# Optimization experiments

Hardware: AMD Instinct MI355X
Metric: run time of the kernel (lower is better)

The kernel has to match this reference:

```python
import jax, jax.numpy as jnp
import numpy as np

N, L, D, H, HIST = 4, 1024, 1024, 16, 128
HD = D // H          # head_dim = 64
SCALE = D ** 0.5     # note: original scales by sqrt(model_dim), not sqrt(head_dim)


def _band_mask():
    # get_mask: tril XOR tril(diag=-history_len) -> True inside the causal band.
    # masked_fill fills where mask is True, so pass the complement (True outside band).
    r = jnp.arange(L)[:, None]
    c = jnp.arange(L)[None, :]
    band = (c <= r) & (c > r - HIST)  # band of width HIST incl. diagonal
    return jnp.broadcast_to(~band, (N, 1, L, L))


def setup_inputs() -> dict:
    key = jax.random.key(0)
    ks = jax.random.split(key, 8)
    s = 0.02
    return {
        "values": jax.random.normal(ks[0], (N, L, D), jnp.float32),
        "keys": jax.random.normal(ks[1], (N, L, D), jnp.float32),
        "query": jax.random.normal(ks[2], (N, L, D), jnp.float32),
        "mask": _band_mask(),
        "Wv": jax.random.normal(ks[3], (HD, HD), jnp.float32) * s,
        "Wk": jax.random.normal(ks[4], (HD, HD), jnp.float32) * s,
        "Wq": jax.random.normal(ks[5], (HD, HD), jnp.float32) * s,
        "Wo": jax.random.normal(ks[6], (D, D), jnp.float32) * s,
        "bo": jax.random.normal(ks[7], (D,), jnp.float32) * s,
    }


def reference(values, keys, query, mask, Wv, Wk, Wq, Wo, bo):
    n, qlen, _ = query.shape
    # split heads and apply per-head linear projections (nn.Linear: x @ W.T)
    v = values.reshape(n, -1, H, HD) @ Wv.T
    k = keys.reshape(n, -1, H, HD) @ Wk.T
    q = query.reshape(n, qlen, H, HD) @ Wq.T
    # full energy [n, h, q, k]
    energy = jnp.einsum('nqhd,nkhd->nhqk', q, k)
    energy = jnp.where(mask, jnp.float32(-1e20), energy)
    scores = jax.nn.softmax(energy / SCALE, axis=-1)
    # NOTE: faithful to original einsum 'nhql,nlhd->nlhd' (reduces over q):
    # attention[n,l,h,d] = (sum_q scores[n,h,q,l]) * v[n,l,h,d]
    attention = jnp.einsum('nhql,nlhd->nlhd', scores, v)
    out = attention.reshape(n, qlen, D) @ Wo.T + bo
    return out
```

## Files before the change

kernel.cpp:

```cpp
#include <hip/hip_runtime.h>
#include <hip/hip_bf16.h>
#include <math.h>


using short8 = __attribute__((ext_vector_type(8))) short;
using f32x4  = __attribute__((ext_vector_type(4))) float;

__device__ __forceinline__ unsigned short f2bf(float x) {
    unsigned u = __float_as_uint(x);
    u += 0x7FFFu + ((u >> 16) & 1u);
    return (unsigned short)(u >> 16);
}

__global__ __launch_bounds__(256) void k_stage(const float* __restrict__ keys,
                                               const float* __restrict__ Wq,
                                               const float* __restrict__ Wk,
                                               const float* __restrict__ Wv,
                                               const float4* __restrict__ Wo4,
                                               unsigned short* __restrict__ kk2p,
                                               ushort4* __restrict__ wob4,
                                               unsigned short* __restrict__ Wvb,
                                               float* __restrict__ w) {
    __shared__ unsigned short Ml[64 * 64];

    const int b = blockIdx.x, tid = threadIdx.x;

    if (b < 1024) {
        const int wv = tid >> 6, lane = tid & 63;
        const int m = lane & 15, q4 = lane >> 4, ksel = q4 * 8;

        {
            short8 aM0, aM1;
#pragma unroll
            for (int j = 0; j < 8; ++j) {
                aM0[j] = (short)f2bf(Wq[(ksel + j) * 64 + wv * 16 + m]);
                aM1[j] = (short)f2bf(Wq[(32 + ksel + j) * 64 + wv * 16 + m]);
            }
#pragma unroll
            for (int fc = 0; fc < 4; ++fc) {
                short8 bM0, bM1;
#pragma unroll
                for (int j = 0; j < 8; ++j) {
                    bM0[j] = (short)f2bf(Wk[(ksel + j) * 64 + fc * 16 + m]);
                    bM1[j] = (short)f2bf(Wk[(32 + ksel + j) * 64 + fc * 16 + m]);
                }
                f32x4 a = f32x4{0.f, 0.f, 0.f, 0.f};
                a = __builtin_amdgcn_mfma_f32_16x16x32_bf16(aM0, bM0, a, 0, 0, 0);
                a = __builtin_amdgcn_mfma_f32_16x16x32_bf16(aM1, bM1, a, 0, 0, 0);
#pragma unroll
                for (int r = 0; r < 4; ++r)
                    Ml[(wv * 16 + q4 * 4 + r) * 64 + fc * 16 + m] =
                        f2bf(a[r] * (1.0f / 32.0f));
            }
        }
        __syncthreads();

        const long R0 = (long)b * 64;
        const float* ka = keys + (R0 + wv * 16 + m) * 64;
        short8 af[2];
#pragma unroll
        for (int ch = 0; ch < 2; ++ch) {
            float4 x0 = *reinterpret_cast<const float4*>(ka + ch * 32 + ksel);
            float4 x1 = *reinterpret_cast<const float4*>(ka + ch * 32 + ksel + 4);
            short8 a;
            a[0] = (short)f2bf(x0.x); a[1] = (short)f2bf(x0.y);
            a[2] = (short)f2bf(x0.z); a[3] = (short)f2bf(x0.w);
            a[4] = (short)f2bf(x1.x); a[5] = (short)f2bf(x1.y);
            a[6] = (short)f2bf(x1.z); a[7] = (short)f2bf(x1.w);
            af[ch] = a;
        }

        f32x4 acc[4];
#pragma unroll
        for (int fc = 0; fc < 4; ++fc) {
            acc[fc] = f32x4{0.f, 0.f, 0.f, 0.f};
#pragma unroll
            for (int ch = 0; ch < 2; ++ch) {
                short8 bf = *reinterpret_cast<const short8*>(
                    &Ml[(fc * 16 + m) * 64 + ch * 32 + ksel]);
                acc[fc] = __builtin_amdgcn_mfma_f32_16x16x32_bf16(af[ch], bf, acc[fc], 0, 0, 0);
            }
        }

        const long rowb = R0 + wv * 16 + (lane >> 4) * 4;
#pragma unroll
        for (int reg = 0; reg < 4; ++reg) {
            long rg = rowb + reg;
            int hh = (int)(rg & 15);
            int ll = (int)((rg >> 4) & 1023);
            int nn = (int)(rg >> 14);
            unsigned short* orow = kk2p + ((size_t)((nn * 16 + hh) * 1024 + ll)) * 64;
#pragma unroll
            for (int fc = 0; fc < 4; ++fc)
                orow[fc * 16 + m] = f2bf(acc[fc][reg]);
        }
    } else if (b < 2048) {
        const int bb = b - 1024;
        int idx = bb * 256 + tid;
        float4 v = Wo4[idx];
        ushort4 o; o.x = f2bf(v.x); o.y = f2bf(v.y);
        o.z = f2bf(v.z); o.w = f2bf(v.w);
        wob4[idx] = o;
        if (bb < 256) w[bb * 256 + tid] = 0.f;
    } else {
        int idx = (b - 2048) * 256 + tid;
        Wvb[idx] = f2bf(Wv[idx]);
    }
}

__global__ __launch_bounds__(256) void k_w2(const float* __restrict__ query,
                                            const unsigned short* __restrict__ kk2p,
                                            float* __restrict__ w) {
    __shared__ float wloc[192];

    const int tid  = threadIdx.x;
    const int b    = blockIdx.x;
    const int nh   = b & 63;
    const int tile = b >> 6;
    const int t0   = tile * 64;
    const int h    = nh & 15, n = nh >> 4;

    if (tid < 192) wloc[tid] = 0.f;
    __syncthreads();

    const int wv = tid >> 6, lane = tid & 63;
    const int m = lane & 15, q4 = lane >> 4, ksel = q4 * 8;

    const float* qrow = query +
        ((size_t)(n * 1024 + t0 + wv * 16 + m)) * 1024 + h * 64;
    float4 x0 = *reinterpret_cast<const float4*>(qrow + ksel);
    float4 x1 = *reinterpret_cast<const float4*>(qrow + ksel + 4);
    float4 x2 = *reinterpret_cast<const float4*>(qrow + 32 + ksel);
    float4 x3 = *reinterpret_cast<const float4*>(qrow + 32 + ksel + 4);
    short8 af0, af1;
    af0[0] = (short)f2bf(x0.x); af0[1] = (short)f2bf(x0.y);
    af0[2] = (short)f2bf(x0.z); af0[3] = (short)f2bf(x0.w);
    af0[4] = (short)f2bf(x1.x); af0[5] = (short)f2bf(x1.y);
    af0[6] = (short)f2bf(x1.z); af0[7] = (short)f2bf(x1.w);
    af1[0] = (short)f2bf(x2.x); af1[1] = (short)f2bf(x2.y);
    af1[2] = (short)f2bf(x2.z); af1[3] = (short)f2bf(x2.w);
    af1[4] = (short)f2bf(x3.x); af1[5] = (short)f2bf(x3.y);
    af1[6] = (short)f2bf(x3.z); af1[7] = (short)f2bf(x3.w);

    const unsigned short* kb = kk2p + (size_t)nh * 1024 * 64;

    f32x4 acc[12];
#pragma unroll
    for (int ni = 0; ni < 12; ++ni) {
        int l = t0 - 127 + ni * 16 + m;
        int lc = min(max(l, 0), 1023);
        const unsigned short* kp = kb + (size_t)lc * 64 + ksel;
        short8 b0 = *reinterpret_cast<const short8*>(kp);
        short8 b1 = *reinterpret_cast<const short8*>(kp + 32);
        f32x4 a = f32x4{0.f, 0.f, 0.f, 0.f};
        a = __builtin_amdgcn_mfma_f32_16x16x32_bf16(af0, b0, a, 0, 0, 0);
        a = __builtin_amdgcn_mfma_f32_16x16x32_bf16(af1, b1, a, 0, 0, 0);
        acc[ni] = a;
    }

    const int rbase = wv * 16 + q4 * 4;
    float rs[4] = {0.f, 0.f, 0.f, 0.f};
#pragma unroll
    for (int ni = 0; ni < 12; ++ni) {
        const int c = ni * 16 + m;
#pragma unroll
        for (int reg = 0; reg < 4; ++reg) {
            const int rlw = rbase + reg;
            bool valid = (c >= rlw) && (c <= rlw + 127) && (c + t0 >= 127);
            float e = valid ? __expf(acc[ni][reg]) : 0.f;
            acc[ni][reg] = e;
            rs[reg] += e;
        }
    }
#pragma unroll
    for (int reg = 0; reg < 4; ++reg) {
#pragma unroll
        for (int mm = 1; mm < 16; mm <<= 1) rs[reg] += __shfl_xor(rs[reg], mm);
        rs[reg] = 1.0f / rs[reg];
    }
#pragma unroll
    for (int ni = 0; ni < 12; ++ni) {
        float cs = acc[ni][0] * rs[0] + acc[ni][1] * rs[1] +
                   acc[ni][2] * rs[2] + acc[ni][3] * rs[3];
        cs += __shfl_xor(cs, 16);
        cs += __shfl_xor(cs, 32);
        if (lane < 16) atomicAdd(&wloc[ni * 16 + m], cs);
    }
    __syncthreads();

    for (int c = tid; c < 192; c += 256) {
        int l = t0 - 127 + c;
        if (l >= 0 && l < 1024)
            atomicAdd(&w[(size_t)nh * 1024 + l], wloc[c]);
    }
}

__global__ __launch_bounds__(256) void k_ap2(const float* __restrict__ values,
                                             const unsigned short* __restrict__ Wvb,
                                             const float* __restrict__ w,
                                             unsigned short* __restrict__ apb) {
    const int tid = threadIdx.x;
    const long R0 = (long)blockIdx.x * 64;
    const int wv = tid >> 6, lane = tid & 63;
    const int m = lane & 15, ksel = (lane >> 4) * 8;

    const float* va = values + (R0 + wv * 16 + m) * 64;
    short8 af[2];
#pragma unroll
    for (int ch = 0; ch < 2; ++ch) {
        float4 x0 = *reinterpret_cast<const float4*>(va + ch * 32 + ksel);
        float4 x1 = *reinterpret_cast<const float4*>(va + ch * 32 + ksel + 4);
        short8 a;
        a[0] = (short)f2bf(x0.x); a[1] = (short)f2bf(x0.y);
        a[2] = (short)f2bf(x0.z); a[3] = (short)f2bf(x0.w);
        a[4] = (short)f2bf(x1.x); a[5] = (short)f2bf(x1.y);
        a[6] = (short)f2bf(x1.z); a[7] = (short)f2bf(x1.w);
        af[ch] = a;
    }

    f32x4 acc[4];
#pragma unroll
    for (int dc = 0; dc < 4; ++dc) {
        acc[dc] = f32x4{0.f, 0.f, 0.f, 0.f};
#pragma unroll
        for (int ch = 0; ch < 2; ++ch) {
            short8 bf = *reinterpret_cast<const short8*>(
                Wvb + (size_t)(dc * 16 + m) * 64 + ch * 32 + ksel);
            acc[dc] = __builtin_amdgcn_mfma_f32_16x16x32_bf16(af[ch], bf, acc[dc], 0, 0, 0);
        }
    }

    const long rowb = R0 + wv * 16 + (lane >> 4) * 4;
    float wf[4];
#pragma unroll
    for (int reg = 0; reg < 4; ++reg) {
        long rg = rowb + reg;
        int hh = (int)(rg & 15);
        int ll = (int)((rg >> 4) & 1023);
        int nn = (int)(rg >> 14);
        wf[reg] = w[((size_t)(nn * 16 + hh) << 10) + ll];
    }
#pragma unroll
    for (int dc = 0; dc < 4; ++dc)
#pragma unroll
        for (int reg = 0; reg < 4; ++reg)
            apb[(size_t)(rowb + reg) * 64 + dc * 16 + m] = f2bf(acc[dc][reg] * wf[reg]);
}

__global__ __launch_bounds__(256) void k_out_mfma(
    const unsigned short* __restrict__ apb,
    const unsigned short* __restrict__ wob,
    const float* __restrict__ bo,
    float* __restrict__ out) {
    __shared__ unsigned short As[2][2][128 * 32];
    __shared__ unsigned short Bs[2][2][64 * 32];

    const int tid  = threadIdx.x;
    const int wv   = tid >> 6;
    const int lane = tid & 63;
    const int m    = lane & 15;

    const int by = blockIdx.x & 31;
    const int bx = blockIdx.x >> 5;
    const long arow0 = (long)by * 128;
    const int  bcol0 = bx * 64;

    f32x4 acc[2][4];
#pragma unroll
    for (int mi = 0; mi < 2; ++mi)
#pragma unroll
        for (int ni = 0; ni < 4; ++ni) acc[mi][ni] = f32x4{0.f, 0.f, 0.f, 0.f};

    const int r0s = tid >> 2;
    const int kks = (tid & 3) * 8;

    auto stage = [&](int buf, int kt) {
        const int k0 = kt * 64;
#pragma unroll
        for (int hh = 0; hh < 2; ++hh) {
            const int kh = k0 + hh * 32;
#pragma unroll
            for (int i = 0; i < 2; ++i) {
                const unsigned short* g =
                    apb + (arow0 + i * 64 + r0s) * 1024 + kh + kks;
                __builtin_amdgcn_global_load_lds(
                    (const __attribute__((address_space(1))) unsigned int*)g,
                    (__attribute__((address_space(3))) unsigned int*)&As[buf][hh][i * 2048 + wv * 512],
                    16, 0, 0);
            }
            {
                const unsigned short* g =
                    wob + (size_t)(bcol0 + r0s) * 1024 + kh + kks;
                __builtin_amdgcn_global_load_lds(
                    (const __attribute__((address_space(1))) unsigned int*)g,
                    (__attribute__((address_space(3))) unsigned int*)&Bs[buf][hh][wv * 512],
                    16, 0, 0);
            }
        }
    };

    stage(0, 0);
    __syncthreads();

    int cur = 0;
    for (int kt = 0; kt < 16; ++kt) {
        if (kt < 15) stage(cur ^ 1, kt + 1);

        const int koff = (lane >> 4) * 8;
        const int rA = wv * 32 + m;
        short8 af[2][2], bf[4][2];
#pragma unroll
        for (int hh = 0; hh < 2; ++hh) {
#pragma unroll
            for (int mi = 0; mi < 2; ++mi)
                af[mi][hh] = *reinterpret_cast<const short8*>(
                    &As[cur][hh][(rA + mi * 16) * 32 + koff]);
#pragma unroll
            for (int ni = 0; ni < 4; ++ni)
                bf[ni][hh] = *reinterpret_cast<const short8*>(
                    &Bs[cur][hh][(ni * 16 + m) * 32 + koff]);
        }
#pragma unroll
        for (int mi = 0; mi < 2; ++mi)
#pragma unroll
            for (int ni = 0; ni < 4; ++ni) {
                acc[mi][ni] = __builtin_amdgcn_mfma_f32_16x16x32_bf16(
                    af[mi][0], bf[ni][0], acc[mi][ni], 0, 0, 0);
                acc[mi][ni] = __builtin_amdgcn_mfma_f32_16x16x32_bf16(
                    af[mi][1], bf[ni][1], acc[mi][ni], 0, 0, 0);
            }
        __syncthreads();
        cur ^= 1;
    }

    const int colb = bcol0 + m;
    const int rowb = (int)arow0 + wv * 32 + (lane >> 4) * 4;
#pragma unroll
    for (int ni = 0; ni < 4; ++ni) {
        const int col = colb + ni * 16;
        const float bias = bo[col];
#pragma unroll
        for (int mi = 0; mi < 2; ++mi) {
            const int row = rowb + mi * 16;
#pragma unroll
            for (int r = 0; r < 4; ++r)
                out[(size_t)(row + r) * 1024 + col] = acc[mi][ni][r] + bias;
        }
    }
}

extern "C" void kernel_launch(void* const* d_in, const int* in_sizes, int n_in,
                              void* d_out, int out_size, void* d_ws, size_t ws_size,
                              hipStream_t stream) {
    const float* values = (const float*)d_in[0];
    const float* keys   = (const float*)d_in[1];
    const float* query  = (const float*)d_in[2];
    const float* Wv     = (const float*)d_in[4];
    const float* Wk     = (const float*)d_in[5];
    const float* Wq     = (const float*)d_in[6];
    const float* Wo     = (const float*)d_in[7];
    const float* bo     = (const float*)d_in[8];
    float* out = (float*)d_out;

    float* w             = (float*)d_ws;
    unsigned short* Wvb  = (unsigned short*)(w + 65536);
    unsigned short* wob  = Wvb + 4096;
    unsigned short* kk2p = wob + 1024 * 1024;
    unsigned short* apb  = kk2p + 64 * 1024 * 64;

    k_stage<<<2064, 256, 0, stream>>>(keys, Wq, Wk, Wv, (const float4*)Wo,
                                      kk2p, (ushort4*)wob, Wvb, w);
    k_w2<<<1024, 256, 0, stream>>>(query, kk2p, w);
    k_ap2<<<1024, 256, 0, stream>>>(values, Wvb, w, apb);
    k_out_mfma<<<512, 256, 0, stream>>>(apb, wob, bo, out);
}
```

Baseline: 156.7 us.

## Fuse key projection into score kernel and replace global atomics with partial sums

Merges the key-projection stage into the attention-weight kernel. Each block now recomputes the projected keys for its 192-row band into shared memory instead of reading a precomputed bf16 key buffer from global memory. Column-sum partials are written per block to a workspace, and the value kernel gathers up to three partials per row, which replaces global atomics and the zeroing pass. This removes one launch and the global round trip for the keys. In exchange, each key row is projected about three times and the block uses more shared memory.

Result: faster. 150.4 us (-4.0%).

```diff
diff --git a/kernel.cpp b/kernel.cpp
--- a/kernel.cpp
+++ b/kernel.cpp
@@ -12,22 +12,36 @@
     return (unsigned short)(u >> 16);
 }
 
-__global__ __launch_bounds__(256) void k_stage(const float* __restrict__ keys,
+__global__ __launch_bounds__(256) void k_fused(const float* __restrict__ keys,
+                                               const float* __restrict__ query,
                                                const float* __restrict__ Wq,
                                                const float* __restrict__ Wk,
                                                const float* __restrict__ Wv,
                                                const float4* __restrict__ Wo4,
-                                               unsigned short* __restrict__ kk2p,
+                                               float* __restrict__ wpart,
                                                ushort4* __restrict__ wob4,
-                                               unsigned short* __restrict__ Wvb,
-                                               float* __restrict__ w) {
+                                               unsigned short* __restrict__ Wvb) {
     __shared__ unsigned short Ml[64 * 64];
+    __shared__ unsigned short band[192 * 72];
+    __shared__ float wloc[192];
 
     const int b = blockIdx.x, tid = threadIdx.x;
 
     if (b < 1024) {
+        const int nh = b & 63, tile = b >> 6;
+        const int t0 = tile * 64;
+        const int h = nh & 15, n = nh >> 4;
         const int wv = tid >> 6, lane = tid & 63;
         const int m = lane & 15, q4 = lane >> 4, ksel = q4 * 8;
+
+        if (tid < 192) wloc[tid] = 0.f;
+
+        const float* qrow = query +
+            ((size_t)(n * 1024 + t0 + wv * 16 + m)) * 1024 + h * 64;
+        const float4 x0 = *reinterpret_cast<const float4*>(qrow + ksel);
+        const float4 x1 = *reinterpret_cast<const float4*>(qrow + ksel + 4);
+        const float4 x2 = *reinterpret_cast<const float4*>(qrow + 32 + ksel);
+        const float4 x3 = *reinterpret_cast<const float4*>(qrow + 32 + ksel + 4);
 
         {
             short8 aM0, aM1;
@@ -55,45 +69,96 @@
         }
         __syncthreads();
 
-        const long R0 = (long)b * 64;
-        const float* ka = keys + (R0 + wv * 16 + m) * 64;
-        short8 af[2];
-#pragma unroll
-        for (int ch = 0; ch < 2; ++ch) {
-            float4 x0 = *reinterpret_cast<const float4*>(ka + ch * 32 + ksel);
-            float4 x1 = *reinterpret_cast<const float4*>(ka + ch * 32 + ksel + 4);
-            short8 a;
-            a[0] = (short)f2bf(x0.x); a[1] = (short)f2bf(x0.y);
-            a[2] = (short)f2bf(x0.z); a[3] = (short)f2bf(x0.w);
-            a[4] = (short)f2bf(x1.x); a[5] = (short)f2bf(x1.y);
-            a[6] = (short)f2bf(x1.z); a[7] = (short)f2bf(x1.w);
-            af[ch] = a;
-        }
-
-        f32x4 acc[4];
-#pragma unroll
-        for (int fc = 0; fc < 4; ++fc) {
-            acc[fc] = f32x4{0.f, 0.f, 0.f, 0.f};
+#pragma unroll
+        for (int grp = 0; grp < 3; ++grp) {
+            const int pA = grp * 64 + wv * 16 + m;
+            const int lrow = min(max(t0 - 127 + pA, 0), 1023);
+            const float* ka = keys + ((size_t)(n * 1024 + lrow)) * 1024 + h * 64;
+            short8 af[2];
 #pragma unroll
             for (int ch = 0; ch < 2; ++ch) {
-                short8 bf = *reinterpret_cast<const short8*>(
-                    &Ml[(fc * 16 + m) * 64 + ch * 32 + ksel]);
-                acc[fc] = __builtin_amdgcn_mfma_f32_16x16x32_bf16(af[ch], bf, acc[fc], 0, 0, 0);
-            }
-        }
-
-        const long rowb = R0 + wv * 16 + (lane >> 4) * 4;
+                float4 k0 = *reinterpret_cast<const float4*>(ka + ch * 32 + ksel);
+                float4 k1 = *reinterpret_cast<const float4*>(ka + ch * 32 + ksel + 4);
+                short8 a;
+                a[0] = (short)f2bf(k0.x); a[1] = (short)f2bf(k0.y);
+                a[2] = (short)f2bf(k0.z); a[3] = (short)f2bf(k0.w);
+                a[4] = (short)f2bf(k1.x); a[5] = (short)f2bf(k1.y);
+                a[6] = (short)f2bf(k1.z); a[7] = (short)f2bf(k1.w);
+                af[ch] = a;
+            }
+            f32x4 acc[4];
+#pragma unroll
+            for (int fc = 0; fc < 4; ++fc) {
+                acc[fc] = f32x4{0.f, 0.f, 0.f, 0.f};
+#pragma unroll
+                for (int ch = 0; ch < 2; ++ch) {
+                    short8 bf = *reinterpret_cast<const short8*>(
+                        &Ml[(fc * 16 + m) * 64 + ch * 32 + ksel]);
+                    acc[fc] = __builtin_amdgcn_mfma_f32_16x16x32_bf16(af[ch], bf, acc[fc], 0, 0, 0);
+                }
+            }
+            const int prow = grp * 64 + wv * 16 + q4 * 4;
+#pragma unroll
+            for (int reg = 0; reg < 4; ++reg)
+#pragma unroll
+                for (int fc = 0; fc < 4; ++fc)
+                    band[(prow + reg) * 72 + fc * 16 + m] = f2bf(acc[fc][reg]);
+        }
+        __syncthreads();
+
+        short8 af0, af1;
+        af0[0] = (short)f2bf(x0.x); af0[1] = (short)f2bf(x0.y);
+        af0[2] = (short)f2bf(x0.z); af0[3] = (short)f2bf(x0.w);
+        af0[4] = (short)f2bf(x1.x); af0[5] = (short)f2bf(x1.y);
+        af0[6] = (short)f2bf(x1.z); af0[7] = (short)f2bf(x1.w);
+        af1[0] = (short)f2bf(x2.x); af1[1] = (short)f2bf(x2.y);
+        af1[2] = (short)f2bf(x2.z); af1[3] = (short)f2bf(x2.w);
+        af1[4] = (short)f2bf(x3.x); af1[5] = (short)f2bf(x3.y);
+        af1[6] = (short)f2bf(x3.z); af1[7] = (short)f2bf(x3.w);
+
+        f32x4 acc[12];
+#pragma unroll
+        for (int ni = 0; ni < 12; ++ni) {
+            const unsigned short* kp_ = &band[(ni * 16 + m) * 72 + ksel];
+            short8 b0 = *reinterpret_cast<const short8*>(kp_);
+            short8 b1 = *reinterpret_cast<const short8*>(kp_ + 32);
+            f32x4 a = f32x4{0.f, 0.f, 0.f, 0.f};
+            a = __builtin_amdgcn_mfma_f32_16x16x32_bf16(af0, b0, a, 0, 0, 0);
+            a = __builtin_amdgcn_mfma_f32_16x16x32_bf16(af1, b1, a, 0, 0, 0);
+            acc[ni] = a;
+        }
+
+        const int rbase = wv * 16 + q4 * 4;
+        float rs[4] = {0.f, 0.f, 0.f, 0.f};
+#pragma unroll
+        for (int ni = 0; ni < 12; ++ni) {
+            const int c = ni * 16 + m;
+#pragma unroll
+            for (int reg = 0; reg < 4; ++reg) {
+                const int rlw = rbase + reg;
+                bool valid = (c >= rlw) && (c <= rlw + 127) && (c + t0 >= 127);
+                float e = valid ? __expf(acc[ni][reg]) : 0.f;
+                acc[ni][reg] = e;
+                rs[reg] += e;
+            }
+        }
 #pragma unroll
         for (int reg = 0; reg < 4; ++reg) {
-            long rg = rowb + reg;
-            int hh = (int)(rg & 15);
-            int ll = (int)((rg >> 4) & 1023);
-            int nn = (int)(rg >> 14);
-            unsigned short* orow = kk2p + ((size_t)((nn * 16 + hh) * 1024 + ll)) * 64;
-#pragma unroll
-            for (int fc = 0; fc < 4; ++fc)
-                orow[fc * 16 + m] = f2bf(acc[fc][reg]);
-        }
+#pragma unroll
+            for (int mm = 1; mm < 16; mm <<= 1) rs[reg] += __shfl_xor(rs[reg], mm);
+            rs[reg] = 1.0f / rs[reg];
+        }
+#pragma unroll
+        for (int ni = 0; ni < 12; ++ni) {
+            float cs = acc[ni][0] * rs[0] + acc[ni][1] * rs[1] +
+                       acc[ni][2] * rs[2] + acc[ni][3] * rs[3];
+            cs += __shfl_xor(cs, 16);
+            cs += __shfl_xor(cs, 32);
+            if (lane < 16) atomicAdd(&wloc[ni * 16 + m], cs);
+        }
+        __syncthreads();
+
+        if (tid < 192) wpart[(size_t)b * 192 + tid] = wloc[tid];
     } else if (b < 2048) {
         const int bb = b - 1024;
         int idx = bb * 256 + tid;
@@ -101,103 +166,15 @@
         ushort4 o; o.x = f2bf(v.x); o.y = f2bf(v.y);
         o.z = f2bf(v.z); o.w = f2bf(v.w);
         wob4[idx] = o;
-        if (bb < 256) w[bb * 256 + tid] = 0.f;
     } else {
         int idx = (b - 2048) * 256 + tid;
         Wvb[idx] = f2bf(Wv[idx]);
     }
 }
 
-__global__ __launch_bounds__(256) void k_w2(const float* __restrict__ query,
-                                            const unsigned short* __restrict__ kk2p,
-                                            float* __restrict__ w) {
-    __shared__ float wloc[192];
-
-    const int tid  = threadIdx.x;
-    const int b    = blockIdx.x;
-    const int nh   = b & 63;
-    const int tile = b >> 6;
-    const int t0   = tile * 64;
-    const int h    = nh & 15, n = nh >> 4;
-
-    if (tid < 192) wloc[tid] = 0.f;
-    __syncthreads();
-
-    const int wv = tid >> 6, lane = tid & 63;
-    const int m = lane & 15, q4 = lane >> 4, ksel = q4 * 8;
-
-    const float* qrow = query +
-        ((size_t)(n * 1024 + t0 + wv * 16 + m)) * 1024 + h * 64;
-    float4 x0 = *reinterpret_cast<const float4*>(qrow + ksel);
-    float4 x1 = *reinterpret_cast<const float4*>(qrow + ksel + 4);
-    float4 x2 = *reinterpret_cast<const float4*>(qrow + 32 + ksel);
-    float4 x3 = *reinterpret_cast<const float4*>(qrow + 32 + ksel + 4);
-    short8 af0, af1;
-    af0[0] = (short)f2bf(x0.x); af0[1] = (short)f2bf(x0.y);
-    af0[2] = (short)f2bf(x0.z); af0[3] = (short)f2bf(x0.w);
-    af0[4] = (short)f2bf(x1.x); af0[5] = (short)f2bf(x1.y);
-    af0[6] = (short)f2bf(x1.z); af0[7] = (short)f2bf(x1.w);
-    af1[0] = (short)f2bf(x2.x); af1[1] = (short)f2bf(x2.y);
-    af1[2] = (short)f2bf(x2.z); af1[3] = (short)f2bf(x2.w);
-    af1[4] = (short)f2bf(x3.x); af1[5] = (short)f2bf(x3.y);
-    af1[6] = (short)f2bf(x3.z); af1[7] = (short)f2bf(x3.w);
-
-    const unsigned short* kb = kk2p + (size_t)nh * 1024 * 64;
-
-    f32x4 acc[12];
-#pragma unroll
-    for (int ni = 0; ni < 12; ++ni) {
-        int l = t0 - 127 + ni * 16 + m;
-        int lc = min(max(l, 0), 1023);
-        const unsigned short* kp = kb + (size_t)lc * 64 + ksel;
-        short8 b0 = *reinterpret_cast<const short8*>(kp);
-        short8 b1 = *reinterpret_cast<const short8*>(kp + 32);
-        f32x4 a = f32x4{0.f, 0.f, 0.f, 0.f};
-        a = __builtin_amdgcn_mfma_f32_16x16x32_bf16(af0, b0, a, 0, 0, 0);
-        a = __builtin_amdgcn_mfma_f32_16x16x32_bf16(af1, b1, a, 0, 0, 0);
-        acc[ni] = a;
-    }
-
-    const int rbase = wv * 16 + q4 * 4;
-    float rs[4] = {0.f, 0.f, 0.f, 0.f};
-#pragma unroll
-    for (int ni = 0; ni < 12; ++ni) {
-        const int c = ni * 16 + m;
-#pragma unroll
-        for (int reg = 0; reg < 4; ++reg) {
-            const int rlw = rbase + reg;
-            bool valid = (c >= rlw) && (c <= rlw + 127) && (c + t0 >= 127);
-            float e = valid ? __expf(acc[ni][reg]) : 0.f;
-            acc[ni][reg] = e;
-            rs[reg] += e;
-        }
-    }
-#pragma unroll
-    for (int reg = 0; reg < 4; ++reg) {
-#pragma unroll
-        for (int mm = 1; mm < 16; mm <<= 1) rs[reg] += __shfl_xor(rs[reg], mm);
-        rs[reg] = 1.0f / rs[reg];
-    }
-#pragma unroll
-    for (int ni = 0; ni < 12; ++ni) {
-        float cs = acc[ni][0] * rs[0] + acc[ni][1] * rs[1] +
-                   acc[ni][2] * rs[2] + acc[ni][3] * rs[3];
-        cs += __shfl_xor(cs, 16);
-        cs += __shfl_xor(cs, 32);
-        if (lane < 16) atomicAdd(&wloc[ni * 16 + m], cs);
-    }
-    __syncthreads();
-
-    for (int c = tid; c < 192; c += 256) {
-        int l = t0 - 127 + c;
-        if (l >= 0 && l < 1024)
-            atomicAdd(&w[(size_t)nh * 1024 + l], wloc[c]);
-    }
-}
-
 __global__ __launch_bounds__(256) void k_ap2(const float* __restrict__ values,
                                              const unsigned short* __restrict__ Wvb,
-                                             const float* __restrict__ w,
+                                             const float* __restrict__ wpart,
                                              unsigned short* __restrict__ apb) {
     const int tid = threadIdx.x;
     const long R0 = (long)blockIdx.x * 64;
@@ -238,7 +215,12 @@
         int hh = (int)(rg & 15);
         int ll = (int)((rg >> 4) & 1023);
         int nn = (int)(rg >> 14);
-        wf[reg] = w[((size_t)(nn * 16 + hh) << 10) + ll];
+        int nhI = nn * 16 + hh;
+        int tmax = min(15, (ll + 127) >> 6);
+        float s = 0.f;
+        for (int t = ll >> 6; t <= tmax; ++t)
+            s += wpart[(size_t)((t << 6) + nhI) * 192 + (ll - (t << 6) + 127)];
+        wf[reg] = s;
     }
 #pragma unroll
     for (int dc = 0; dc < 4; ++dc)
@@ -362,15 +344,13 @@
     const float* bo     = (const float*)d_in[8];
     float* out = (float*)d_out;
 
-    float* w             = (float*)d_ws;
-    unsigned short* Wvb  = (unsigned short*)(w + 65536);
+    float* wpart         = (float*)d_ws;
+    unsigned short* Wvb  = (unsigned short*)(wpart + 196608);
     unsigned short* wob  = Wvb + 4096;
-    unsigned short* kk2p = wob + 1024 * 1024;
-    unsigned short* apb  = kk2p + 64 * 1024 * 64;
-
-    k_stage<<<2064, 256, 0, stream>>>(keys, Wq, Wk, Wv, (const float4*)Wo,
-                                      kk2p, (ushort4*)wob, Wvb, w);
-    k_w2<<<1024, 256, 0, stream>>>(query, kk2p, w);
-    k_ap2<<<1024, 256, 0, stream>>>(values, Wvb, w, apb);
+    unsigned short* apb  = wob + 1024 * 1024;
+
+    k_fused<<<2064, 256, 0, stream>>>(keys, query, Wq, Wk, Wv, (const float4*)Wo,
+                                      wpart, (ushort4*)wob, Wvb);
+    k_ap2<<<1024, 256, 0, stream>>>(values, Wvb, wpart, apb);
     k_out_mfma<<<512, 256, 0, stream>>>(apb, wob, bo, out);
 }
```
